# Optimization experiments

Hardware: AMD Instinct MI355X
Metric: run time of the kernel (lower is better)

The kernel has to match this reference:

```python
import jax, jax.numpy as jnp
import numpy as np
from jax import lax

B, T, I, H, L, C = 256, 512, 128, 256, 2, 10


def _lstm_layer(x_tm, lengths, W_ih, W_hh, b_ih, b_hh):
    # x_tm: [T, B, in]; lengths: [B]
    b = b_ih + b_hh  # [4H]
    h0 = jnp.zeros((x_tm.shape[1], H), x_tm.dtype)
    c0 = jnp.zeros_like(h0)

    def step(carry, inp):
        h, c = carry
        x_t, t = inp
        gates = x_t @ W_ih.T + h @ W_hh.T + b  # [B, 4H]
        i, f, g, o = jnp.split(gates, 4, axis=-1)
        i = jax.nn.sigmoid(i); f = jax.nn.sigmoid(f)
        g = jnp.tanh(g);        o = jax.nn.sigmoid(o)
        c_new = f * c + i * g
        h_new = o * jnp.tanh(c_new)
        m = (t < lengths)[:, None]  # freeze state past each sequence's length
        h = jnp.where(m, h_new, h)
        c = jnp.where(m, c_new, c)
        return (h, c), h

    (hT, cT), h_seq = lax.scan(step, (h0, c0), (x_tm, jnp.arange(x_tm.shape[0])))
    return h_seq, hT


def setup_inputs() -> dict:
    key = jax.random.key(0)
    ks = jax.random.split(key, 16)
    s_i = 1.0 / np.sqrt(H)
    inp = {
        'x': jax.random.normal(ks[0], (B, T, I), jnp.float32),
        'lengths': jax.random.randint(ks[1], (B,), 1, T + 1),
        'W_fc': jax.random.uniform(ks[2], (C, H), jnp.float32, -s_i, s_i),
        'b_fc': jax.random.uniform(ks[3], (C,), jnp.float32, -s_i, s_i),
    }
    for l in range(L):
        in_dim = I if l == 0 else H
        k0, k1, k2, k3 = jax.random.split(jax.random.fold_in(key, 100 + l), 4)
        inp[f'W_ih_{l}'] = jax.random.uniform(k0, (4 * H, in_dim), jnp.float32, -s_i, s_i)
        inp[f'W_hh_{l}'] = jax.random.uniform(k1, (4 * H, H), jnp.float32, -s_i, s_i)
        inp[f'b_ih_{l}'] = jax.random.uniform(k2, (4 * H,), jnp.float32, -s_i, s_i)
        inp[f'b_hh_{l}'] = jax.random.uniform(k3, (4 * H,), jnp.float32, -s_i, s_i)
    return inp


def reference(x, lengths, W_fc, b_fc,
              W_ih_0, W_hh_0, b_ih_0, b_hh_0,
              W_ih_1, W_hh_1, b_ih_1, b_hh_1):
    layer_params = [(W_ih_0, W_hh_0, b_ih_0, b_hh_0),
                    (W_ih_1, W_hh_1, b_ih_1, b_hh_1)]
    seq = jnp.swapaxes(x, 0, 1)  # [T, B, I] time-major
    hT = None
    for (W_ih, W_hh, b_ih, b_hh) in layer_params:
        seq, hT = _lstm_layer(seq, lengths, W_ih, W_hh, b_ih, b_hh)
    logits = hT @ W_fc.T + b_fc  # final hidden state of last layer
    return jax.nn.softmax(logits, axis=1)
```

## Files before the change

kernel.cpp:

```cpp
#include <hip/hip_runtime.h>

#define TT 512
#define BB 256
#define II 128
#define HH 256
#define CC 10

typedef __attribute__((ext_vector_type(8))) _Float16 f16x8;
typedef __attribute__((ext_vector_type(4))) _Float16 f16x4;
typedef __attribute__((ext_vector_type(4))) float    f32x4;

__device__ __forceinline__ float fsig(float x){ return 1.0f/(1.0f+__expf(-x)); }
__device__ __forceinline__ float ftanh(float x){ return 2.0f/(1.0f+__expf(-2.0f*x)) - 1.0f; }

__device__ __forceinline__ unsigned cpoll(unsigned* p){
  return __hip_atomic_fetch_add(p, 0u, __ATOMIC_RELAXED, __HIP_MEMORY_SCOPE_AGENT);
}
__device__ __forceinline__ unsigned poll_until(unsigned* p, unsigned tgt){
  unsigned v = 0;
  if((threadIdx.x & 63) == 0){
    v = cpoll(p);
    while(v < tgt){ __builtin_amdgcn_s_sleep(2); v = cpoll(p); }
  }
  unsigned u = __builtin_amdgcn_readfirstlane(v);
  asm volatile("" ::: "memory");
  return u;
}
__device__ __forceinline__ void store_h16(_Float16* p, _Float16 v){
  unsigned b32 = (unsigned)__builtin_bit_cast(unsigned short, v);
  asm volatile("global_store_short %0, %1, off sc0 sc1" :: "v"(p), "v"(b32) : "memory");
}
__device__ __forceinline__ f16x8 load_sc(const _Float16* p){
  f16x8 r;
  asm volatile("global_load_dwordx4 %0, %1, off sc0 sc1" : "=v"(r) : "v"(p) : "memory");
  return r;
}
#define PIN(x) asm volatile("" : "+v"(x))

template<int KXT, bool IS_L1>
__device__ __forceinline__ void run_wave(
    const _Float16* __restrict__ xin,
    const _Float16* __restrict__ Wh,
    const _Float16* __restrict__ Wx,
    const float* __restrict__ b_ih, const float* __restrict__ b_hh,
    const int* __restrict__ lengths,
    _Float16* __restrict__ hbuf,
    float* __restrict__ hT,
    unsigned* cown, unsigned* cprod, int gb, int gj)
{
  constexpr int KXV = KXT*32;
  const int lane = threadIdx.x & 63;
  const int quad = lane >> 4;
  const int l15  = lane & 15;
  const int koff = quad << 3;
  const int b0   = gb << 4;
  const int u    = (gj << 4) + l15;

  f16x8 wh[4][8], wx[4][KXT];
  float bias[4];
#pragma unroll
  for(int g=0; g<4; ++g){
    const int row = g*HH + u;
#pragma unroll
    for(int kt=0; kt<8; ++kt){
      wh[g][kt] = *(const f16x8*)(Wh + (size_t)row*HH + kt*32 + koff);
      PIN(wh[g][kt]);
    }
#pragma unroll
    for(int kt=0; kt<KXT; ++kt){
      wx[g][kt] = *(const f16x8*)(Wx + (size_t)row*KXV + kt*32 + koff);
      PIN(wx[g][kt]);
    }
    bias[g] = b_ih[row] + b_hh[row];
  }

  int sb[4], len[4]; float cs[4], hs[4];
#pragma unroll
  for(int r=0; r<4; ++r){
    sb[r]  = b0 + (quad<<2) + r;
    len[r] = lengths[sb[r]];
    cs[r] = 0.f; hs[r] = 0.f;
  }

  unsigned lastp = 0, lasto = 0;

  f16x8 axn[KXT];
  if(!IS_L1){
    const _Float16* xp = xin + ((size_t)(b0+l15)*TT + 0)*KXV + koff;
#pragma unroll
    for(int kt=0; kt<KXT; ++kt) axn[kt] = *(const f16x8*)(xp + kt*32);
  }

  for(int t=0; t<TT; ++t){
    f16x8 ax[KXT];
    if(IS_L1){
      const unsigned tgtp = 16u*(unsigned)(t+1);
      if(lastp < tgtp) lastp = poll_until(cprod, tgtp);
      const _Float16* xp = xin + ((size_t)t*BB + b0 + l15)*HH + koff;
#pragma unroll
      for(int kt=0; kt<KXT; ++kt) ax[kt] = *(const f16x8*)(xp + kt*32);
    } else {
#pragma unroll
      for(int kt=0; kt<KXT; ++kt) ax[kt] = axn[kt];
    }

    if(t > 0){
      const unsigned tgto = 16u*(unsigned)t;
      if(lasto < tgto) lasto = poll_until(cown, tgto);
    }
    f16x8 ah[8];
    if(t > 0){
      if(IS_L1){
        const _Float16* hp = hbuf + (((size_t)((t-1)&3))*BB + b0 + l15)*HH + koff;
#pragma unroll
        for(int kt=0; kt<8; ++kt) ah[kt] = load_sc(hp + kt*32);
      } else {
        const _Float16* hp = hbuf + ((size_t)(t-1)*BB + b0 + l15)*HH + koff;
#pragma unroll
        for(int kt=0; kt<8; ++kt) ah[kt] = *(const f16x8*)(hp + kt*32);
      }
    }

    f32x4 acc[4];
#pragma unroll
    for(int g=0; g<4; ++g) acc[g] = (f32x4){bias[g],bias[g],bias[g],bias[g]};
#pragma unroll
    for(int kt=0; kt<KXT; ++kt)
#pragma unroll
      for(int g=0; g<4; ++g)
        acc[g] = __builtin_amdgcn_mfma_f32_16x16x32_f16(ax[kt], wx[g][kt], acc[g], 0,0,0);

    if(t > 0){
      if(IS_L1){
        asm volatile("s_waitcnt vmcnt(0)"
          : "+v"(ah[0]),"+v"(ah[1]),"+v"(ah[2]),"+v"(ah[3]),
            "+v"(ah[4]),"+v"(ah[5]),"+v"(ah[6]),"+v"(ah[7]) :: "memory");
      }
#pragma unroll
      for(int kt=0; kt<8; ++kt)
#pragma unroll
        for(int g=0; g<4; ++g)
          acc[g] = __builtin_amdgcn_mfma_f32_16x16x32_f16(ah[kt], wh[g][kt], acc[g], 0,0,0);
    }

#pragma unroll
    for(int r=0; r<4; ++r){
      float iv = fsig (acc[0][r]);
      float fv = fsig (acc[1][r]);
      float gv = ftanh(acc[2][r]);
      float ov = fsig (acc[3][r]);
      float cn = fv*cs[r] + iv*gv;
      float hn = ov*ftanh(cn);
      if(t < len[r]){ cs[r] = cn; hs[r] = hn; }
      _Float16* hp = IS_L1
        ? hbuf + (((size_t)(t&3))*BB + sb[r])*HH + u
        : hbuf + ((size_t)t*BB + sb[r])*HH + u;
      store_h16(hp, (_Float16)hs[r]);
      if(IS_L1 && t == TT-1) hT[(size_t)sb[r]*HH + u] = hs[r];
    }

    asm volatile("s_waitcnt vmcnt(0)" ::: "memory");
    if(lane == 0)
      __hip_atomic_fetch_add(cown, 1u, __ATOMIC_RELAXED, __HIP_MEMORY_SCOPE_AGENT);

    if(!IS_L1 && t+1 < TT){
      const _Float16* xp = xin + ((size_t)(b0+l15)*TT + (t+1))*KXV + koff;
#pragma unroll
      for(int kt=0; kt<KXT; ++kt) axn[kt] = *(const f16x8*)(xp + kt*32);
    }
  }
}

__global__ __launch_bounds__(64, 1)
void lstm_fused(const _Float16* __restrict__ xc,
                const _Float16* __restrict__ Wh0, const _Float16* __restrict__ Wx0,
                const _Float16* __restrict__ Wh1, const _Float16* __restrict__ Wx1,
                const float* __restrict__ b_ih0, const float* __restrict__ b_hh0,
                const float* __restrict__ b_ih1, const float* __restrict__ b_hh1,
                const int* __restrict__ lens,
                _Float16* __restrict__ h0seq, _Float16* __restrict__ h1ring,
                float* __restrict__ hT, unsigned* __restrict__ ctr)
{
  const int blk   = blockIdx.x;
  const int layer = blk >> 8;
  const int gb    = blk & 15;
  const int gj    = (blk >> 4) & 15;
  unsigned* c0 = ctr + gb*32;
  unsigned* c1 = ctr + (16+gb)*32;
  if(layer == 0){
    run_wave<4,false>(xc, Wh0, Wx0, b_ih0, b_hh0, lens, h0seq, nullptr,
                      c0, nullptr, gb, gj);
  } else {
    run_wave<8,true >(h0seq, Wh1, Wx1, b_ih1, b_hh1, lens, h1ring, hT,
                      c1, c0, gb, gj);
  }
}

__global__ __launch_bounds__(256)
void cvt4(const float* __restrict__ in, _Float16* __restrict__ out, int n4)
{
  int i = blockIdx.x*256 + threadIdx.x;
  if(i < n4){
    float4 v = ((const float4*)in)[i];
    f16x4 o;
    o[0]=(_Float16)v.x; o[1]=(_Float16)v.y; o[2]=(_Float16)v.z; o[3]=(_Float16)v.w;
    ((f16x4*)out)[i] = o;
  }
}

__global__ __launch_bounds__(64)
void fc_softmax(const float* __restrict__ hT,
                const float* __restrict__ W_fc,
                const float* __restrict__ b_fc,
                float* __restrict__ out)
{
  const int b = blockIdx.x;
  const int lane = threadIdx.x;
  float p[CC];
#pragma unroll
  for (int c = 0; c < CC; ++c) p[c] = 0.f;
  const float* hb = hT + b * HH;
  for (int k = lane; k < HH; k += 64){
    float hv = hb[k];
#pragma unroll
    for (int c = 0; c < CC; ++c) p[c] += hv * W_fc[c * HH + k];
  }
#pragma unroll
  for (int c = 0; c < CC; ++c){
#pragma unroll
    for (int off = 32; off > 0; off >>= 1) p[c] += __shfl_down(p[c], off);
  }
  if (lane == 0){
    float m = -1e30f;
#pragma unroll
    for (int c = 0; c < CC; ++c){ p[c] += b_fc[c]; m = fmaxf(m, p[c]); }
    float ssum = 0.f;
#pragma unroll
    for (int c = 0; c < CC; ++c){ p[c] = __expf(p[c] - m); ssum += p[c]; }
    float inv = 1.0f / ssum;
#pragma unroll
    for (int c = 0; c < CC; ++c) out[b * CC + c] = p[c] * inv;
  }
}

extern "C" void kernel_launch(void* const* d_in, const int* in_sizes, int n_in,
                              void* d_out, int out_size, void* d_ws, size_t ws_size,
                              hipStream_t stream) {
  const float* x      = (const float*)d_in[0];
  const int*   lens   = (const int*)  d_in[1];
  const float* W_fc   = (const float*)d_in[2];
  const float* b_fc   = (const float*)d_in[3];
  const float* W_ih0  = (const float*)d_in[4];
  const float* W_hh0  = (const float*)d_in[5];
  const float* b_ih0  = (const float*)d_in[6];
  const float* b_hh0  = (const float*)d_in[7];
  const float* W_ih1  = (const float*)d_in[8];
  const float* W_hh1  = (const float*)d_in[9];
  const float* b_ih1  = (const float*)d_in[10];
  const float* b_hh1  = (const float*)d_in[11];
  float* out = (float*)d_out;

  char* ws = (char*)d_ws;
  unsigned* ctr  = (unsigned*)ws;
  float*    hT   = (float*)(ws + 8192);
  _Float16* Wh0c = (_Float16*)(ws + 270336);
  _Float16* Wx0c = (_Float16*)(ws + 794624);
  _Float16* Wh1c = (_Float16*)(ws + 1056768);
  _Float16* Wx1c = (_Float16*)(ws + 1581056);
  _Float16* xc   = (_Float16*)(ws + 2105344);
  _Float16* h0   = (_Float16*)(ws + 35659776);
  _Float16* h1r  = (_Float16*)(ws + 102768640);

  hipMemsetAsync(ws, 0, 8192, stream);

  cvt4<<<dim3((BB*TT*II/4 + 255)/256), dim3(256), 0, stream>>>(x,     xc,   BB*TT*II/4);
  cvt4<<<dim3((4*HH*HH/4  + 255)/256), dim3(256), 0, stream>>>(W_hh0, Wh0c, 4*HH*HH/4);
  cvt4<<<dim3((4*HH*II/4  + 255)/256), dim3(256), 0, stream>>>(W_ih0, Wx0c, 4*HH*II/4);
  cvt4<<<dim3((4*HH*HH/4  + 255)/256), dim3(256), 0, stream>>>(W_hh1, Wh1c, 4*HH*HH/4);
  cvt4<<<dim3((4*HH*HH/4  + 255)/256), dim3(256), 0, stream>>>(W_ih1, Wx1c, 4*HH*HH/4);

  lstm_fused<<<dim3(512), dim3(64), 0, stream>>>(
      xc, Wh0c, Wx0c, Wh1c, Wx1c, b_ih0, b_hh0, b_ih1, b_hh1, lens,
      h0, h1r, hT, ctr);

  fc_softmax<<<dim3(BB), dim3(64), 0, stream>>>(hT, W_fc, b_fc, out);
}
```

Measured before the change: 1.758 ms.

## Replace counter polling with step-tagged hidden-state rings for LSTM inter-wave sync

Hidden-state values are now stored as 32-bit words, each holding the fp16 value plus a 16-bit timestep tag. Consumers spin-read the data until every tag matches, so they no longer poll a per-group counter before loading. Layer 0 writes to a 4-slot ring instead of the full sequence buffer, and layer 1 uses a 2-slot ring. Back-pressure is one counter per batch group that layer 1 increments after consuming a slot. This is meant to take the counter round-trip and store-fence latency off the serial recurrence critical path, at the cost of doubled hidden-state traffic, retry loops and the extra tag-check permute work.

```diff
diff --git a/kernel.cpp b/kernel.cpp
--- a/kernel.cpp
+++ b/kernel.cpp
@@ -10,6 +10,9 @@
 typedef __attribute__((ext_vector_type(4))) _Float16 f16x4;
 typedef __attribute__((ext_vector_type(4))) float    f32x4;
 
+#define SELLO 0x05040100u
+#define SELHI 0x07060302u
+
 __device__ __forceinline__ float fsig(float x){ return 1.0f/(1.0f+__expf(-x)); }
 __device__ __forceinline__ float ftanh(float x){ return 2.0f/(1.0f+__expf(-2.0f*x)) - 1.0f; }
 
@@ -20,41 +23,64 @@
   unsigned v = 0;
   if((threadIdx.x & 63) == 0){
     v = cpoll(p);
-    while(v < tgt){ __builtin_amdgcn_s_sleep(2); v = cpoll(p); }
+    while(v < tgt){ __builtin_amdgcn_s_sleep(1); v = cpoll(p); }
   }
   unsigned u = __builtin_amdgcn_readfirstlane(v);
   asm volatile("" ::: "memory");
   return u;
 }
-__device__ __forceinline__ void store_h16(_Float16* p, _Float16 v){
-  unsigned b32 = (unsigned)__builtin_bit_cast(unsigned short, v);
-  asm volatile("global_store_short %0, %1, off sc0 sc1" :: "v"(p), "v"(b32) : "memory");
-}
-__device__ __forceinline__ f16x8 load_sc(const _Float16* p){
+
+__device__ __forceinline__ void ld2(const unsigned* p, uint4& a, uint4& b){
+  asm volatile("global_load_dwordx4 %0, %2, off sc0 sc1\n\t"
+               "global_load_dwordx4 %1, %2, off offset:16 sc0 sc1"
+               : "=&v"(a), "=&v"(b) : "v"(p) : "memory");
+}
+__device__ __forceinline__ f16x8 ld1h(const _Float16* p){
   f16x8 r;
   asm volatile("global_load_dwordx4 %0, %1, off sc0 sc1" : "=v"(r) : "v"(p) : "memory");
   return r;
 }
-#define PIN(x) asm volatile("" : "+v"(x))
-
-template<int KXT, bool IS_L1>
+__device__ __forceinline__ void waitv0 (){ asm volatile("s_waitcnt vmcnt(0)"  ::: "memory"); }
+__device__ __forceinline__ void waitv4 (){ asm volatile("s_waitcnt vmcnt(4)"  ::: "memory"); }
+__device__ __forceinline__ void waitv16(){ asm volatile("s_waitcnt vmcnt(16)" ::: "memory"); }
+#define PIN4(vv) asm volatile("" : "+v"((vv).x), "+v"((vv).y), "+v"((vv).z), "+v"((vv).w))
+#define PINH(vv) asm volatile("" : "+v"(vv))
+
+__device__ __forceinline__ void store_u32(unsigned* p, unsigned w){
+  asm volatile("global_store_dword %0, %1, off sc0 sc1" :: "v"(p), "v"(w) : "memory");
+}
+__device__ __forceinline__ unsigned tagbad(const uint4& a, unsigned dup){
+  return (__builtin_amdgcn_perm(a.y, a.x, SELHI) ^ dup)
+       | (__builtin_amdgcn_perm(a.w, a.z, SELHI) ^ dup);
+}
+__device__ __forceinline__ f16x8 extr8(const uint4& a, const uint4& b){
+  union { unsigned d[4]; f16x8 v; } r;
+  r.d[0] = __builtin_amdgcn_perm(a.y, a.x, SELLO);
+  r.d[1] = __builtin_amdgcn_perm(a.w, a.z, SELLO);
+  r.d[2] = __builtin_amdgcn_perm(b.y, b.x, SELLO);
+  r.d[3] = __builtin_amdgcn_perm(b.w, b.z, SELLO);
+  return r.v;
+}
+
+template<bool IS_L1>
 __device__ __forceinline__ void run_wave(
-    const _Float16* __restrict__ xin,
-    const _Float16* __restrict__ Wh,
-    const _Float16* __restrict__ Wx,
+    const _Float16* __restrict__ xc,
+    unsigned* __restrict__ ring0,
+    const _Float16* __restrict__ Wh, const _Float16* __restrict__ Wx,
     const float* __restrict__ b_ih, const float* __restrict__ b_hh,
     const int* __restrict__ lengths,
-    _Float16* __restrict__ hbuf,
+    unsigned* __restrict__ ring1,
     float* __restrict__ hT,
-    unsigned* cown, unsigned* cprod, int gb, int gj)
+    unsigned* __restrict__ ctrX, int gb, int gj)
 {
-  constexpr int KXV = KXT*32;
+  constexpr int KXT = IS_L1 ? 8 : 4;
   const int lane = threadIdx.x & 63;
   const int quad = lane >> 4;
   const int l15  = lane & 15;
   const int koff = quad << 3;
   const int b0   = gb << 4;
   const int u    = (gj << 4) + l15;
+  const size_t arow = (size_t)(b0 + l15);
 
   f16x8 wh[4][8], wx[4][KXT];
   float bias[4];
@@ -64,12 +90,12 @@
 #pragma unroll
     for(int kt=0; kt<8; ++kt){
       wh[g][kt] = *(const f16x8*)(Wh + (size_t)row*HH + kt*32 + koff);
-      PIN(wh[g][kt]);
+      PINH(wh[g][kt]);
     }
 #pragma unroll
     for(int kt=0; kt<KXT; ++kt){
-      wx[g][kt] = *(const f16x8*)(Wx + (size_t)row*KXV + kt*32 + koff);
-      PIN(wx[g][kt]);
+      wx[g][kt] = *(const f16x8*)(Wx + (size_t)row*(KXT*32) + kt*32 + koff);
+      PINH(wx[g][kt]);
     }
     bias[g] = b_ih[row] + b_hh[row];
   }
@@ -82,45 +108,51 @@
     cs[r] = 0.f; hs[r] = 0.f;
   }
 
-  unsigned lastp = 0, lasto = 0;
-
-  f16x8 axn[KXT];
-  if(!IS_L1){
-    const _Float16* xp = xin + ((size_t)(b0+l15)*TT + 0)*KXV + koff;
-#pragma unroll
-    for(int kt=0; kt<KXT; ++kt) axn[kt] = *(const f16x8*)(xp + kt*32);
-  }
-
-  for(int t=0; t<TT; ++t){
-    f16x8 ax[KXT];
-    if(IS_L1){
-      const unsigned tgtp = 16u*(unsigned)(t+1);
-      if(lastp < tgtp) lastp = poll_until(cprod, tgtp);
-      const _Float16* xp = xin + ((size_t)t*BB + b0 + l15)*HH + koff;
-#pragma unroll
-      for(int kt=0; kt<KXT; ++kt) ax[kt] = *(const f16x8*)(xp + kt*32);
-    } else {
-#pragma unroll
-      for(int kt=0; kt<KXT; ++kt) ax[kt] = axn[kt];
-    }
-
-    if(t > 0){
-      const unsigned tgto = 16u*(unsigned)t;
-      if(lasto < tgto) lasto = poll_until(cown, tgto);
-    }
-    f16x8 ah[8];
-    if(t > 0){
-      if(IS_L1){
-        const _Float16* hp = hbuf + (((size_t)((t-1)&3))*BB + b0 + l15)*HH + koff;
-#pragma unroll
-        for(int kt=0; kt<8; ++kt) ah[kt] = load_sc(hp + kt*32);
-      } else {
-        const _Float16* hp = hbuf + ((size_t)(t-1)*BB + b0 + l15)*HH + koff;
-#pragma unroll
-        for(int kt=0; kt<8; ++kt) ah[kt] = *(const f16x8*)(hp + kt*32);
-      }
-    }
-
+  unsigned bp = 0;
+  f16x8 ax[KXT];
+
+  if(IS_L1){
+    uint4 xr[16];
+    const unsigned* xp = ring0 + arow*HH + koff;
+#pragma unroll
+    for(int kt=0; kt<8; ++kt) ld2(xp + kt*32, xr[2*kt], xr[2*kt+1]);
+    const unsigned dupx = 1u | (1u<<16);
+    for(;;){
+      waitv0();
+#pragma unroll
+      for(int i=0; i<16; ++i) PIN4(xr[i]);
+      unsigned bad = 0;
+#pragma unroll
+      for(int i=0; i<16; ++i) bad |= tagbad(xr[i], dupx);
+      if(__all(bad == 0)) break;
+#pragma unroll
+      for(int kt=0; kt<8; ++kt) ld2(xp + kt*32, xr[2*kt], xr[2*kt+1]);
+    }
+    if(lane == 0)
+      __hip_atomic_fetch_add(ctrX, 1u, __ATOMIC_RELAXED, __HIP_MEMORY_SCOPE_AGENT);
+#pragma unroll
+    for(int kt=0; kt<8; ++kt) ax[kt] = extr8(xr[2*kt], xr[2*kt+1]);
+  } else {
+    const _Float16* xp = xc + (arow*TT + 0)*II + koff;
+#pragma unroll
+    for(int kt=0; kt<KXT; ++kt) ax[kt] = ld1h(xp + kt*32);
+  }
+
+  for(int s=0; s<TT; ++s){
+    uint4 hr[16];
+    const int rslot = IS_L1 ? ((s-1)&1) : ((s-1)&3);
+    const unsigned* hp = (IS_L1 ? ring1 : ring0)
+                       + ((size_t)rslot*BB + arow)*HH + koff;
+    if(s > 0){
+#pragma unroll
+      for(int kt=0; kt<8; ++kt) ld2(hp + kt*32, hr[2*kt], hr[2*kt+1]);
+    }
+
+    if(!IS_L1){
+      if(s > 0) waitv16(); else waitv0();
+#pragma unroll
+      for(int kt=0; kt<KXT; ++kt) PINH(ax[kt]);
+    }
     f32x4 acc[4];
 #pragma unroll
     for(int g=0; g<4; ++g) acc[g] = (f32x4){bias[g],bias[g],bias[g],bias[g]};
@@ -130,19 +162,44 @@
       for(int g=0; g<4; ++g)
         acc[g] = __builtin_amdgcn_mfma_f32_16x16x32_f16(ax[kt], wx[g][kt], acc[g], 0,0,0);
 
-    if(t > 0){
-      if(IS_L1){
-        asm volatile("s_waitcnt vmcnt(0)"
-          : "+v"(ah[0]),"+v"(ah[1]),"+v"(ah[2]),"+v"(ah[3]),
-            "+v"(ah[4]),"+v"(ah[5]),"+v"(ah[6]),"+v"(ah[7]) :: "memory");
+    uint4 xr[16];
+    bool xr_live = false;
+    if(s > 0){
+      const unsigned dup = (unsigned)s | ((unsigned)s << 16);
+      for(;;){
+        waitv0();
+#pragma unroll
+        for(int i=0; i<16; ++i) PIN4(hr[i]);
+        unsigned bad = 0;
+#pragma unroll
+        for(int i=0; i<16; ++i) bad |= tagbad(hr[i], dup);
+        if(__all(bad == 0)) break;
+#pragma unroll
+        for(int kt=0; kt<8; ++kt) ld2(hp + kt*32, hr[2*kt], hr[2*kt+1]);
+      }
+      f16x8 ah[8];
+#pragma unroll
+      for(int kt=0; kt<8; ++kt) ah[kt] = extr8(hr[2*kt], hr[2*kt+1]);
+
+      if(IS_L1 && s+1 < TT){
+        const unsigned* xp = ring0 + ((size_t)((s+1)&3)*BB + arow)*HH + koff;
+#pragma unroll
+        for(int kt=0; kt<8; ++kt) ld2(xp + kt*32, xr[2*kt], xr[2*kt+1]);
+        xr_live = true;
       }
 #pragma unroll
       for(int kt=0; kt<8; ++kt)
 #pragma unroll
         for(int g=0; g<4; ++g)
           acc[g] = __builtin_amdgcn_mfma_f32_16x16x32_f16(ah[kt], wh[g][kt], acc[g], 0,0,0);
-    }
-
+    } else if(IS_L1){
+      const unsigned* xp = ring0 + ((size_t)1*BB + arow)*HH + koff;
+#pragma unroll
+      for(int kt=0; kt<8; ++kt) ld2(xp + kt*32, xr[2*kt], xr[2*kt+1]);
+      xr_live = true;
+    }
+
+    unsigned hw[4];
 #pragma unroll
     for(int r=0; r<4; ++r){
       float iv = fsig (acc[0][r]);
@@ -151,22 +208,59 @@
       float ov = fsig (acc[3][r]);
       float cn = fv*cs[r] + iv*gv;
       float hn = ov*ftanh(cn);
-      if(t < len[r]){ cs[r] = cn; hs[r] = hn; }
-      _Float16* hp = IS_L1
-        ? hbuf + (((size_t)(t&3))*BB + sb[r])*HH + u
-        : hbuf + ((size_t)t*BB + sb[r])*HH + u;
-      store_h16(hp, (_Float16)hs[r]);
-      if(IS_L1 && t == TT-1) hT[(size_t)sb[r]*HH + u] = hs[r];
-    }
-
-    asm volatile("s_waitcnt vmcnt(0)" ::: "memory");
-    if(lane == 0)
-      __hip_atomic_fetch_add(cown, 1u, __ATOMIC_RELAXED, __HIP_MEMORY_SCOPE_AGENT);
-
-    if(!IS_L1 && t+1 < TT){
-      const _Float16* xp = xin + ((size_t)(b0+l15)*TT + (t+1))*KXV + koff;
-#pragma unroll
-      for(int kt=0; kt<KXT; ++kt) axn[kt] = *(const f16x8*)(xp + kt*32);
+      if(s < len[r]){ cs[r] = cn; hs[r] = hn; }
+      _Float16 hf = (_Float16)hs[r];
+      hw[r] = (unsigned)__builtin_bit_cast(unsigned short, hf);
+    }
+
+    if(!IS_L1 && s >= 4){
+      const unsigned tgt = 16u*(unsigned)(s-3);
+      if(bp < tgt) bp = poll_until(ctrX, tgt);
+    }
+
+    {
+      const int wslot = IS_L1 ? (s&1) : (s&3);
+      const unsigned tw = ((unsigned)(s+1)) << 16;
+      unsigned* op = (IS_L1 ? ring1 : ring0) + (size_t)wslot*BB*HH + u;
+#pragma unroll
+      for(int r=0; r<4; ++r)
+        store_u32(op + (size_t)sb[r]*HH, tw | hw[r]);
+    }
+    if(IS_L1 && s == TT-1){
+#pragma unroll
+      for(int r=0; r<4; ++r) hT[(size_t)sb[r]*HH + u] = hs[r];
+    }
+
+    if(s+1 < TT){
+      if(IS_L1){
+        const unsigned* xp = ring0 + ((size_t)((s+1)&3)*BB + arow)*HH + koff;
+        const unsigned dupx = (unsigned)(s+2) | ((unsigned)(s+2) << 16);
+        if(!xr_live){
+#pragma unroll
+          for(int kt=0; kt<8; ++kt) ld2(xp + kt*32, xr[2*kt], xr[2*kt+1]);
+        }
+        bool first = true;
+        for(;;){
+          if(first) waitv4(); else waitv0();
+          first = false;
+#pragma unroll
+          for(int i=0; i<16; ++i) PIN4(xr[i]);
+          unsigned bad = 0;
+#pragma unroll
+          for(int i=0; i<16; ++i) bad |= tagbad(xr[i], dupx);
+          if(__all(bad == 0)) break;
+#pragma unroll
+          for(int kt=0; kt<8; ++kt) ld2(xp + kt*32, xr[2*kt], xr[2*kt+1]);
+        }
+        if(lane == 0)
+          __hip_atomic_fetch_add(ctrX, 1u, __ATOMIC_RELAXED, __HIP_MEMORY_SCOPE_AGENT);
+#pragma unroll
+        for(int kt=0; kt<8; ++kt) ax[kt] = extr8(xr[2*kt], xr[2*kt+1]);
+      } else {
+        const _Float16* xp = xc + (arow*TT + (s+1))*II + koff;
+#pragma unroll
+        for(int kt=0; kt<KXT; ++kt) ax[kt] = ld1h(xp + kt*32);
+      }
     }
   }
 }
@@ -178,21 +272,20 @@
                 const float* __restrict__ b_ih0, const float* __restrict__ b_hh0,
                 const float* __restrict__ b_ih1, const float* __restrict__ b_hh1,
                 const int* __restrict__ lens,
-                _Float16* __restrict__ h0seq, _Float16* __restrict__ h1ring,
+                unsigned* __restrict__ ring0, unsigned* __restrict__ ring1,
                 float* __restrict__ hT, unsigned* __restrict__ ctr)
 {
   const int blk   = blockIdx.x;
   const int layer = blk >> 8;
   const int gb    = blk & 15;
   const int gj    = (blk >> 4) & 15;
-  unsigned* c0 = ctr + gb*32;
-  unsigned* c1 = ctr + (16+gb)*32;
+  unsigned* cx = ctr + gb*32;
   if(layer == 0){
-    run_wave<4,false>(xc, Wh0, Wx0, b_ih0, b_hh0, lens, h0seq, nullptr,
-                      c0, nullptr, gb, gj);
+    run_wave<false>(xc, ring0, Wh0, Wx0, b_ih0, b_hh0, lens,
+                    nullptr, nullptr, cx, gb, gj);
   } else {
-    run_wave<8,true >(h0seq, Wh1, Wx1, b_ih1, b_hh1, lens, h1ring, hT,
-                      c1, c0, gb, gj);
+    run_wave<true >(nullptr, ring0, Wh1, Wx1, b_ih1, b_hh1, lens,
+                    ring1, hT, cx, gb, gj);
   }
 }
 
@@ -261,17 +354,17 @@
   float* out = (float*)d_out;
 
   char* ws = (char*)d_ws;
-  unsigned* ctr  = (unsigned*)ws;
-  float*    hT   = (float*)(ws + 8192);
-  _Float16* Wh0c = (_Float16*)(ws + 270336);
-  _Float16* Wx0c = (_Float16*)(ws + 794624);
-  _Float16* Wh1c = (_Float16*)(ws + 1056768);
-  _Float16* Wx1c = (_Float16*)(ws + 1581056);
-  _Float16* xc   = (_Float16*)(ws + 2105344);
-  _Float16* h0   = (_Float16*)(ws + 35659776);
-  _Float16* h1r  = (_Float16*)(ws + 102768640);
-
-  hipMemsetAsync(ws, 0, 8192, stream);
+  unsigned* ctr   = (unsigned*)ws;
+  unsigned* ring0 = (unsigned*)(ws + 8192);
+  unsigned* ring1 = (unsigned*)(ws + 1056768);
+  float*    hT    = (float*)(ws + 1581056);
+  _Float16* Wh0c  = (_Float16*)(ws + 1843200);
+  _Float16* Wx0c  = (_Float16*)(ws + 2367488);
+  _Float16* Wh1c  = (_Float16*)(ws + 2629632);
+  _Float16* Wx1c  = (_Float16*)(ws + 3153920);
+  _Float16* xc    = (_Float16*)(ws + 3678208);
+
+  (void)hipMemsetAsync(ws, 0, 1581056, stream);
 
   cvt4<<<dim3((BB*TT*II/4 + 255)/256), dim3(256), 0, stream>>>(x,     xc,   BB*TT*II/4);
   cvt4<<<dim3((4*HH*HH/4  + 255)/256), dim3(256), 0, stream>>>(W_hh0, Wh0c, 4*HH*HH/4);
@@ -281,7 +374,7 @@
 
   lstm_fused<<<dim3(512), dim3(64), 0, stream>>>(
       xc, Wh0c, Wx0c, Wh1c, Wx1c, b_ih0, b_hh0, b_ih1, b_hh1, lens,
-      h0, h1r, hT, ctr);
+      ring0, ring1, hT, ctr);
 
   fc_softmax<<<dim3(BB), dim3(64), 0, stream>>>(hT, W_fc, b_fc, out);
 }
```

Measured after the change: 6.059 ms. +244.6%, slower.
